# Optimization experiments

Measured on AMD Instinct MI355X. Metric: run time of the kernel, lower is better.

The kernel has to match this reference:

```python
import jax, jax.numpy as jnp
import numpy as np

B, N, D, OUT = 8, 2048, 128, 128

def setup_inputs() -> dict:
    key = jax.random.key(0)
    k1, k2, k3, k4 = jax.random.split(key, 4)
    input_ = jax.random.normal(k1, (B, N, D), dtype=jnp.float32)
    adj_matrix = jax.random.randint(k2, (B, N, N), 0, 2, dtype=jnp.int32)
    W = jax.random.normal(k3, (2 * D, OUT), dtype=jnp.float32) * 0.05
    b = jax.random.normal(k4, (OUT,), dtype=jnp.float32) * 0.05
    return {"input_": input_, "adj_matrix": adj_matrix, "W": W, "b": b}

def reference(input_, adj_matrix, W, b):
    adj = adj_matrix.astype(jnp.float32)           # [B,N,N]
    deg = jnp.sum(adj, axis=2)                     # [B,N]
    deg = jnp.where(deg == 0, 1.0, deg)
    agg = jnp.einsum('bnm,bmd->bnd', adj, input_) / deg[:, :, None]  # mean aggregation
    feat = jnp.concatenate([input_, agg], axis=2)  # [B,N,2D]
    out = jax.nn.sigmoid(feat @ W + b)             # [B,N,OUT]
    out = out / jnp.linalg.norm(out, axis=2, keepdims=True)
    return out
```

## Files before the change

### kernel.cpp

```cpp
#include <hip/hip_runtime.h>

#define Bn 8
#define Nn 2048
#define Dn 128
#define OUTn 128

typedef __attribute__((ext_vector_type(8))) short bf16x8;
typedef __attribute__((ext_vector_type(8))) unsigned short ushort8;
typedef __attribute__((ext_vector_type(4))) float f32x4;
typedef __attribute__((ext_vector_type(4))) int int4v;
typedef __attribute__((ext_vector_type(4))) unsigned int uint4v;
typedef __attribute__((ext_vector_type(4))) float float4v;

__device__ __forceinline__ unsigned short f2bf(float f) {
  unsigned int u = __builtin_bit_cast(unsigned int, f);
  u += 0x7FFFu + ((u >> 16) & 1u);
  return (unsigned short)(u >> 16);
}

__global__ __launch_bounds__(256) void gcn_prep(const float* __restrict__ in,
                                                const float* __restrict__ W,
                                                unsigned short* __restrict__ inT,
                                                unsigned short* __restrict__ WT) {
  const int tid = threadIdx.x;
  if (blockIdx.x >= 256) {
    int gid = (blockIdx.x - 256) * 256 + tid;
    int j = gid >> 8, k = gid & 255;
    WT[gid] = f2bf(W[k * OUTn + j]);
    return;
  }
  const int b = blockIdx.x >> 5;
  const int n0 = (blockIdx.x & 31) * 64;
  __shared__ __attribute__((aligned(16))) unsigned short lds[64][130];
  #pragma unroll
  for (int c = 0; c < 32; ++c) {
    int e = tid + c * 256;
    int i = e >> 7, d = e & 127;
    lds[i][d] = f2bf(in[((size_t)(b * Nn + n0 + i)) * Dn + d]);
  }
  __syncthreads();
  #pragma unroll
  for (int c = 0; c < 4; ++c) {
    int ch = tid + c * 256;
    int d = ch >> 3, g = (ch & 7) * 8;
    ushort8 v;
    #pragma unroll
    for (int e = 0; e < 8; ++e) v[e] = lds[g + e][d];
    *(ushort8*)(inT + ((size_t)(b * Dn + d)) * Nn + n0 + g) = v;
  }
}

union SMem {
  struct {
    int A[3][32][64];
    unsigned short Bs[3][128][64];
  } s;
  struct {
    unsigned short aggl[32][136];
    float rowsum[32][4];
    float degs[32];
  } e;
};

#define STAGE(cur, kt) do {                                                    \
    {                                                                          \
      const int r_ = wv * 4 + (l >> 4);                                        \
      const int cg_ = (l & 15) ^ (r_ & 7);                                     \
      const int* gsrc_ = adjB + (size_t)r_ * Nn + (kt) * 64 + cg_ * 4;         \
      __builtin_amdgcn_global_load_lds(                                        \
          (const __attribute__((address_space(1))) void*)gsrc_,                \
          (__attribute__((address_space(3))) void*)(smc + (cur) * 8192 +       \
                                                   wv * 1024),                 \
          16, 0, 0);                                                           \
    }                                                                          \
    _Pragma("unroll")                                                          \
    for (int c_ = 0; c_ < 2; ++c_) {                                           \
      const int d_ = c_ * 64 + wv * 8 + (l >> 3);                              \
      const int cg_ = (l & 7) ^ (d_ & 7);                                      \
      const unsigned short* gsrc_ = inTb + (size_t)d_ * Nn + (kt) * 64 + cg_ * 8; \
      __builtin_amdgcn_global_load_lds(                                        \
          (const __attribute__((address_space(1))) void*)gsrc_,                \
          (__attribute__((address_space(3))) void*)(smc + 24576 +              \
                                                   (cur) * 16384 +             \
                                                   c_ * 8192 + wv * 1024),     \
          16, 0, 0);                                                           \
    }                                                                          \
  } while (0)

#define COMPUTE(cur) do {                                                      \
    const char* Abase = smc + (cur) * 8192 + (rg * 16 + lr) * 256;             \
    const char* Bbase = smc + 24576 + (cur) * 16384 + (ch * 32 + lr) * 128;    \
    _Pragma("unroll")                                                          \
    for (int kc = 0; kc < 2; ++kc) {                                           \
      const int c0_ = kc * 8 + lg * 2;                                         \
      int4v ai0 = *(const int4v*)(Abase + ((c0_ ^ swz8) * 16));                \
      int4v ai1 = *(const int4v*)(Abase + (((c0_ + 1) ^ swz8) * 16));          \
      dsum += ai0[0] + ai0[1] + ai0[2] + ai0[3] +                              \
              ai1[0] + ai1[1] + ai1[2] + ai1[3];                               \
      uint4v aw;                                                               \
      aw[0] = (unsigned)ai0[0] * 0x3F80u + (unsigned)ai0[1] * 0x3F800000u;     \
      aw[1] = (unsigned)ai0[2] * 0x3F80u + (unsigned)ai0[3] * 0x3F800000u;     \
      aw[2] = (unsigned)ai1[0] * 0x3F80u + (unsigned)ai1[1] * 0x3F800000u;     \
      aw[3] = (unsigned)ai1[2] * 0x3F80u + (unsigned)ai1[3] * 0x3F800000u;     \
      bf16x8 af = __builtin_bit_cast(bf16x8, aw);                              \
      _Pragma("unroll")                                                        \
      for (int cf = 0; cf < 2; ++cf) {                                         \
        bf16x8 bfm = *(const bf16x8*)(Bbase + (size_t)cf * 16 * 128 +          \
                                      (((kc * 4 + lg) ^ swz8) * 16));          \
        acc[cf] = __builtin_amdgcn_mfma_f32_16x16x32_bf16(af, bfm, acc[cf],    \
                                                          0, 0, 0);            \
      }                                                                        \
    }                                                                          \
  } while (0)

#define WAITBAR(N) do {                                                        \
    asm volatile("s_waitcnt vmcnt(" #N ")" ::: "memory");                      \
    __builtin_amdgcn_s_barrier();                                              \
    __builtin_amdgcn_sched_barrier(0);                                         \
  } while (0)

__global__ __launch_bounds__(512, 4) void gcn_main(
    const float* __restrict__ input_, const int* __restrict__ adj,
    const float* __restrict__ bvec, const unsigned short* __restrict__ inT,
    const unsigned short* __restrict__ WT, float* __restrict__ out) {
  __shared__ SMem sm;
  char* smc = (char*)&sm;
  const int tid = threadIdx.x;
  const int wv = tid >> 6;
  const int l = tid & 63, lr = l & 15, lg = (l >> 4) & 3;
  const int rg = wv >> 2, ch = wv & 3;

  const int swz = (blockIdx.x & 7) * 64 + (blockIdx.x >> 3);
  const int bb = swz >> 6;
  const int row0 = (swz & 63) * 32;
  const int grow0 = bb * Nn + row0;

  const int* adjB = adj + (size_t)grow0 * Nn;
  const unsigned short* inTb = inT + (size_t)bb * Dn * Nn;

  const int swz8 = lr & 7;
  f32x4 acc[2] = {};
  int dsum = 0;

  STAGE(0, 0);
  STAGE(1, 1);

  #pragma unroll 1
  for (int j = 0; j < 10; ++j) {
    const int kt = 3 * j; (void)kt;
    WAITBAR(3); STAGE(2, kt + 2); COMPUTE(0);
    WAITBAR(3); STAGE(0, kt + 3); COMPUTE(1);
    WAITBAR(3); STAGE(1, kt + 4); COMPUTE(2);
  }
  WAITBAR(3); COMPUTE(0);
  WAITBAR(0); COMPUTE(1);

  __syncthreads();

  {
    int s = dsum;
    s += __shfl_xor(s, 16);
    s += __shfl_xor(s, 32);
    if (l < 16) sm.e.degs[rg * 16 + l] = (s == 0) ? 1.0f : (float)s;
  }
  __syncthreads();

  float dgi[4];
  #pragma unroll
  for (int reg = 0; reg < 4; ++reg)
    dgi[reg] = 1.0f / sm.e.degs[rg * 16 + lg * 4 + reg];
  #pragma unroll
  for (int cf = 0; cf < 2; ++cf)
    #pragma unroll
    for (int reg = 0; reg < 4; ++reg)
      sm.e.aggl[rg * 16 + lg * 4 + reg][ch * 32 + cf * 16 + lr] =
          f2bf(acc[cf][reg] * dgi[reg]);
  __syncthreads();

  f32x4 acc2[2] = {};
  const float* xrow = input_ + (size_t)(grow0 + rg * 16 + lr) * Dn;
  #pragma unroll
  for (int ks = 0; ks < 8; ++ks) {
    bf16x8 af;
    if (ks < 4) {
      float4v f0 = *(const float4v*)(xrow + ks * 32 + lg * 8);
      float4v f1 = *(const float4v*)(xrow + ks * 32 + lg * 8 + 4);
      ushort8 vv;
      #pragma unroll
      for (int e = 0; e < 4; ++e) { vv[e] = f2bf(f0[e]); vv[e + 4] = f2bf(f1[e]); }
      af = __builtin_bit_cast(bf16x8, vv);
    } else {
      af = *(const bf16x8*)&sm.e.aggl[rg * 16 + lr][(ks - 4) * 32 + lg * 8];
    }
    #pragma unroll
    for (int cf = 0; cf < 2; ++cf) {
      bf16x8 bw = *(const bf16x8*)(WT + (size_t)(ch * 32 + cf * 16 + lr) * 256 +
                                   ks * 32 + lg * 8);
      acc2[cf] = __builtin_amdgcn_mfma_f32_16x16x32_bf16(af, bw, acc2[cf], 0, 0, 0);
    }
  }

  float bcol[2];
  bcol[0] = bvec[ch * 32 + lr];
  bcol[1] = bvec[ch * 32 + 16 + lr];
  float sg[2][4];
  #pragma unroll
  for (int cf = 0; cf < 2; ++cf)
    #pragma unroll
    for (int reg = 0; reg < 4; ++reg) {
      float x = acc2[cf][reg] + bcol[cf];
      sg[cf][reg] = 1.0f / (1.0f + expf(-x));
    }
  #pragma unroll
  for (int reg = 0; reg < 4; ++reg) {
    float p = sg[0][reg] * sg[0][reg] + sg[1][reg] * sg[1][reg];
    p += __shfl_xor(p, 1);
    p += __shfl_xor(p, 2);
    p += __shfl_xor(p, 4);
    p += __shfl_xor(p, 8);
    if (lr == 0) sm.e.rowsum[rg * 16 + lg * 4 + reg][ch] = p;
  }
  __syncthreads();
  #pragma unroll
  for (int reg = 0; reg < 4; ++reg) {
    const int row = rg * 16 + lg * 4 + reg;
    float nrm = rsqrtf(sm.e.rowsum[row][0] + sm.e.rowsum[row][1] +
                       sm.e.rowsum[row][2] + sm.e.rowsum[row][3]);
    #pragma unroll
    for (int cf = 0; cf < 2; ++cf)
      out[(size_t)(grow0 + row) * OUTn + ch * 32 + cf * 16 + lr] =
          sg[cf][reg] * nrm;
  }
}

extern "C" void kernel_launch(void* const* d_in, const int* in_sizes, int n_in,
                              void* d_out, int out_size, void* d_ws, size_t ws_size,
                              hipStream_t stream) {
  (void)in_sizes; (void)n_in; (void)out_size; (void)ws_size;
  const float* input_ = (const float*)d_in[0];
  const int* adj = (const int*)d_in[1];
  const float* W = (const float*)d_in[2];
  const float* bvec = (const float*)d_in[3];
  float* out = (float*)d_out;

  unsigned short* inT = (unsigned short*)d_ws;
  unsigned short* WT = inT + (size_t)Bn * Dn * Nn;

  hipLaunchKernelGGL(gcn_prep, dim3(384), dim3(256), 0, stream, input_, W, inT, WT);
  hipLaunchKernelGGL(gcn_main, dim3(512), dim3(512), 0, stream,
                     input_, adj, bvec, inT, WT, out);
}
```

Measured before the change: 45.22 us.

## Halve row tile to 16 rows per block and deepen pipeline to four stages

```diff
diff --git a/kernel.cpp b/kernel.cpp
--- a/kernel.cpp
+++ b/kernel.cpp
@@ -52,13 +52,13 @@
 
 union SMem {
   struct {
-    int A[3][32][64];
-    unsigned short Bs[3][128][64];
+    int A[4][16][64];
+    unsigned short Bs[4][128][64];
   } s;
   struct {
-    unsigned short aggl[32][136];
-    float rowsum[32][4];
-    float degs[32];
+    unsigned short aggl[16][136];
+    float rowsum[16][4];
+    float degs[16];
   } e;
 };
 
@@ -69,27 +69,27 @@
       const int* gsrc_ = adjB + (size_t)r_ * Nn + (kt) * 64 + cg_ * 4;         \
       __builtin_amdgcn_global_load_lds(                                        \
           (const __attribute__((address_space(1))) void*)gsrc_,                \
-          (__attribute__((address_space(3))) void*)(smc + (cur) * 8192 +       \
+          (__attribute__((address_space(3))) void*)(smc + (cur) * 4096 +       \
                                                    wv * 1024),                 \
           16, 0, 0);                                                           \
     }                                                                          \
     _Pragma("unroll")                                                          \
-    for (int c_ = 0; c_ < 2; ++c_) {                                           \
-      const int d_ = c_ * 64 + wv * 8 + (l >> 3);                              \
+    for (int c_ = 0; c_ < 4; ++c_) {                                           \
+      const int d_ = wv * 32 + c_ * 8 + (l >> 3);                              \
       const int cg_ = (l & 7) ^ (d_ & 7);                                      \
       const unsigned short* gsrc_ = inTb + (size_t)d_ * Nn + (kt) * 64 + cg_ * 8; \
       __builtin_amdgcn_global_load_lds(                                        \
           (const __attribute__((address_space(1))) void*)gsrc_,                \
-          (__attribute__((address_space(3))) void*)(smc + 24576 +              \
+          (__attribute__((address_space(3))) void*)(smc + 16384 +              \
                                                    (cur) * 16384 +             \
-                                                   c_ * 8192 + wv * 1024),     \
+                                                   wv * 4096 + c_ * 1024),     \
           16, 0, 0);                                                           \
     }                                                                          \
   } while (0)
 
 #define COMPUTE(cur) do {                                                      \
-    const char* Abase = smc + (cur) * 8192 + (rg * 16 + lr) * 256;             \
-    const char* Bbase = smc + 24576 + (cur) * 16384 + (ch * 32 + lr) * 128;    \
+    const char* Abase = smc + (cur) * 4096 + lr * 256;                         \
+    const char* Bbase = smc + 16384 + (cur) * 16384 + (wv * 32 + lr) * 128;    \
     _Pragma("unroll")                                                          \
     for (int kc = 0; kc < 2; ++kc) {                                           \
       const int c0_ = kc * 8 + lg * 2;                                         \
@@ -119,7 +119,7 @@
     __builtin_amdgcn_sched_barrier(0);                                         \
   } while (0)
 
-__global__ __launch_bounds__(512, 4) void gcn_main(
+__global__ __launch_bounds__(256, 2) void gcn_main(
     const float* __restrict__ input_, const int* __restrict__ adj,
     const float* __restrict__ bvec, const unsigned short* __restrict__ inT,
     const unsigned short* __restrict__ WT, float* __restrict__ out) {
@@ -128,11 +128,10 @@
   const int tid = threadIdx.x;
   const int wv = tid >> 6;
   const int l = tid & 63, lr = l & 15, lg = (l >> 4) & 3;
-  const int rg = wv >> 2, ch = wv & 3;
-
-  const int swz = (blockIdx.x & 7) * 64 + (blockIdx.x >> 3);
-  const int bb = swz >> 6;
-  const int row0 = (swz & 63) * 32;
+
+  const int swz = (blockIdx.x & 7) * 128 + (blockIdx.x >> 3);
+  const int bb = swz >> 7;
+  const int row0 = (swz & 127) * 16;
   const int grow0 = bb * Nn + row0;
 
   const int* adjB = adj + (size_t)grow0 * Nn;
@@ -144,16 +143,20 @@
 
   STAGE(0, 0);
   STAGE(1, 1);
+  STAGE(2, 2);
 
   #pragma unroll 1
-  for (int j = 0; j < 10; ++j) {
-    const int kt = 3 * j; (void)kt;
-    WAITBAR(3); STAGE(2, kt + 2); COMPUTE(0);
-    WAITBAR(3); STAGE(0, kt + 3); COMPUTE(1);
-    WAITBAR(3); STAGE(1, kt + 4); COMPUTE(2);
-  }
-  WAITBAR(3); COMPUTE(0);
-  WAITBAR(0); COMPUTE(1);
+  for (int j = 0; j < 7; ++j) {
+    const int kt = 4 * j;
+    WAITBAR(10); STAGE(3, kt + 3); COMPUTE(0);
+    WAITBAR(10); STAGE(0, kt + 4); COMPUTE(1);
+    WAITBAR(10); STAGE(1, kt + 5); COMPUTE(2);
+    WAITBAR(10); STAGE(2, kt + 6); COMPUTE(3);
+  }
+  WAITBAR(10); STAGE(3, 31); COMPUTE(0);
+  WAITBAR(10); COMPUTE(1);
+  WAITBAR(5);  COMPUTE(2);
+  WAITBAR(0);  COMPUTE(3);
 
   __syncthreads();
 
@@ -161,24 +164,24 @@
     int s = dsum;
     s += __shfl_xor(s, 16);
     s += __shfl_xor(s, 32);
-    if (l < 16) sm.e.degs[rg * 16 + l] = (s == 0) ? 1.0f : (float)s;
+    if (l < 16) sm.e.degs[l] = (s == 0) ? 1.0f : (float)s;
   }
   __syncthreads();
 
   float dgi[4];
   #pragma unroll
   for (int reg = 0; reg < 4; ++reg)
-    dgi[reg] = 1.0f / sm.e.degs[rg * 16 + lg * 4 + reg];
+    dgi[reg] = 1.0f / sm.e.degs[lg * 4 + reg];
   #pragma unroll
   for (int cf = 0; cf < 2; ++cf)
     #pragma unroll
     for (int reg = 0; reg < 4; ++reg)
-      sm.e.aggl[rg * 16 + lg * 4 + reg][ch * 32 + cf * 16 + lr] =
+      sm.e.aggl[lg * 4 + reg][wv * 32 + cf * 16 + lr] =
           f2bf(acc[cf][reg] * dgi[reg]);
   __syncthreads();
 
   f32x4 acc2[2] = {};
-  const float* xrow = input_ + (size_t)(grow0 + rg * 16 + lr) * Dn;
+  const float* xrow = input_ + (size_t)(grow0 + lr) * Dn;
   #pragma unroll
   for (int ks = 0; ks < 8; ++ks) {
     bf16x8 af;
@@ -190,19 +193,19 @@
       for (int e = 0; e < 4; ++e) { vv[e] = f2bf(f0[e]); vv[e + 4] = f2bf(f1[e]); }
       af = __builtin_bit_cast(bf16x8, vv);
     } else {
-      af = *(const bf16x8*)&sm.e.aggl[rg * 16 + lr][(ks - 4) * 32 + lg * 8];
+      af = *(const bf16x8*)&sm.e.aggl[lr][(ks - 4) * 32 + lg * 8];
     }
     #pragma unroll
     for (int cf = 0; cf < 2; ++cf) {
-      bf16x8 bw = *(const bf16x8*)(WT + (size_t)(ch * 32 + cf * 16 + lr) * 256 +
+      bf16x8 bw = *(const bf16x8*)(WT + (size_t)(wv * 32 + cf * 16 + lr) * 256 +
                                    ks * 32 + lg * 8);
       acc2[cf] = __builtin_amdgcn_mfma_f32_16x16x32_bf16(af, bw, acc2[cf], 0, 0, 0);
     }
   }
 
   float bcol[2];
-  bcol[0] = bvec[ch * 32 + lr];
-  bcol[1] = bvec[ch * 32 + 16 + lr];
+  bcol[0] = bvec[wv * 32 + lr];
+  bcol[1] = bvec[wv * 32 + 16 + lr];
   float sg[2][4];
   #pragma unroll
   for (int cf = 0; cf < 2; ++cf)
@@ -218,17 +221,17 @@
     p += __shfl_xor(p, 2);
     p += __shfl_xor(p, 4);
     p += __shfl_xor(p, 8);
-    if (lr == 0) sm.e.rowsum[rg * 16 + lg * 4 + reg][ch] = p;
+    if (lr == 0) sm.e.rowsum[lg * 4 + reg][wv] = p;
   }
   __syncthreads();
   #pragma unroll
   for (int reg = 0; reg < 4; ++reg) {
-    const int row = rg * 16 + lg * 4 + reg;
+    const int row = lg * 4 + reg;
     float nrm = rsqrtf(sm.e.rowsum[row][0] + sm.e.rowsum[row][1] +
                        sm.e.rowsum[row][2] + sm.e.rowsum[row][3]);
     #pragma unroll
     for (int cf = 0; cf < 2; ++cf)
-      out[(size_t)(grow0 + row) * OUTn + ch * 32 + cf * 16 + lr] =
+      out[(size_t)(grow0 + row) * OUTn + wv * 32 + cf * 16 + lr] =
           sg[cf][reg] * nrm;
   }
 }
@@ -247,6 +250,6 @@
   unsigned short* WT = inT + (size_t)Bn * Dn * Nn;
 
   hipLaunchKernelGGL(gcn_prep, dim3(384), dim3(256), 0, stream, input_, W, inT, WT);
-  hipLaunchKernelGGL(gcn_main, dim3(512), dim3(512), 0, stream,
+  hipLaunchKernelGGL(gcn_main, dim3(1024), dim3(256), 0, stream,
                      input_, adj, bvec, inT, WT, out);
 }
```

Result: slower. 54.62 us (+20.8%).
